# Performance work log

Hardware: AMD Instinct MI355X
Metric: run time of the kernel (lower is better)

## Reference

```python
import jax, jax.numpy as jnp
import numpy as np

M = 262144          # total lanes
N_GROUPS = 32768    # unique obstacle ids (static; original uses torch.unique)
H = 64              # lane_hidden_size
I = 64              # lane_info_enc_size
F = 64              # lane_future_enc_size
SOFT_ARGMAX_DEGREE = 1.0


def setup_inputs() -> dict:
    key = jax.random.key(0)
    k = jax.random.split(key, 8)
    lane_ht = jax.random.normal(k[0], (M, H), jnp.float32)
    lane_info_enc = jax.random.normal(k[1], (M, I), jnp.float32)
    lane_future_enc = jax.random.normal(k[2], (M, F), jnp.float32)
    # sorted group ids covering every group (8 lanes per obstacle)
    same_obstacle_mask = jnp.sort(jnp.arange(M, dtype=jnp.int32) % N_GROUPS).reshape(M, 1)
    # lane_scoring_mlp params: Linear(128->16) + ReLU + Linear(16->1)
    W1 = jax.random.normal(k[3], (H + I, 16), jnp.float32) * 0.05
    b1 = jnp.zeros((16,), jnp.float32)
    W2 = jax.random.normal(k[4], (16, 1), jnp.float32) * 0.05
    b2 = jnp.zeros((1,), jnp.float32)
    return {"lane_ht": lane_ht, "lane_info_enc": lane_info_enc,
            "lane_future_enc": lane_future_enc,
            "W1": W1, "b1": b1, "W2": W2, "b2": b2,
            "same_obstacle_mask": same_obstacle_mask}


def reference(lane_ht, lane_info_enc, lane_future_enc, W1, b1, W2, b2, same_obstacle_mask):
    seg = same_obstacle_mask.reshape(-1)                       # [M] int group ids
    # per-lane score via small MLP
    x = jnp.concatenate([lane_ht, lane_info_enc], axis=1)      # [M, 128]
    h = jax.nn.relu(x @ W1 + b1)                               # [M, 16]
    score = (h @ W2 + b2).reshape(-1) * SOFT_ARGMAX_DEGREE     # [M]
    # per-group (segment) softmax -- exact math of the dense MxN min/max/exp/sum emulation
    smax = jax.lax.stop_gradient(
        jax.ops.segment_max(score, seg, num_segments=N_GROUPS))  # [N]
    e = jnp.exp(score - smax[seg])                             # [M]
    denom = jax.ops.segment_sum(e, seg, num_segments=N_GROUPS)  # [N]
    prob = e / denom[seg]                                      # [M]
    # softmax-weighted per-group pooling of concatenated encodings
    total = jnp.concatenate([lane_ht, lane_info_enc, lane_future_enc], axis=1)  # [M, 192]
    return jax.ops.segment_sum(total * prob[:, None], seg, num_segments=N_GROUPS)  # [N, 192]
```

## Files before the change

kernel.cpp:

```cpp
#include <hip/hip_runtime.h>


__global__ __launch_bounds__(128, 8) void lane_attn_kernel(
    const float* __restrict__ ht,
    const float* __restrict__ info,
    const float* __restrict__ fut,
    const float* __restrict__ W1,
    const float* __restrict__ b1,
    const float* __restrict__ W2,
    const float* __restrict__ b2,
    const int*   __restrict__ seg,
    float*       __restrict__ out)
{
    const int t    = threadIdx.x & 63;
    const int w    = __builtin_amdgcn_readfirstlane(threadIdx.x >> 6);
    const int base = blockIdx.x * 64;

    __shared__ float hpart[2][64][17];

    float h[16];
#pragma unroll
    for (int j = 0; j < 16; ++j) h[j] = w ? 0.0f : b1[j];

    const float*  src = w ? info : ht;
    const float*  w1  = W1 + w * (64 * 16);
    const float4* p   = (const float4*)(src + (size_t)(base + t) * 64);

#pragma unroll 8
    for (int k4 = 0; k4 < 16; ++k4) {
        float4 v = p[k4];
#pragma unroll
        for (int j = 0; j < 16; ++j) {
            h[j] = fmaf(v.x, w1[(k4 * 4 + 0) * 16 + j], h[j]);
            h[j] = fmaf(v.y, w1[(k4 * 4 + 1) * 16 + j], h[j]);
            h[j] = fmaf(v.z, w1[(k4 * 4 + 2) * 16 + j], h[j]);
            h[j] = fmaf(v.w, w1[(k4 * 4 + 3) * 16 + j], h[j]);
        }
    }

#pragma unroll
    for (int j = 0; j < 16; ++j) hpart[w][t][j] = h[j];
    __syncthreads();

    const int lr = w * 32 + (t & 31);
    float score = b2[0];
#pragma unroll
    for (int j = 0; j < 16; ++j) {
        const float hj = hpart[0][lr][j] + hpart[1][lr][j];
        score = fmaf(fmaxf(hj, 0.0f), W2[j], score);
    }

    float m = score;
    m = fmaxf(m, __shfl_xor(m, 1));
    m = fmaxf(m, __shfl_xor(m, 2));
    m = fmaxf(m, __shfl_xor(m, 4));
    float e = __expf(score - m);
    float s = e;
    s += __shfl_xor(s, 1);
    s += __shfl_xor(s, 2);
    s += __shfl_xor(s, 4);
    const float prob = e / s;

    const int c = t;
    for (int gg = 0; gg < 4; ++gg) {
        const int r0  = base + w * 32 + gg * 8;
        const int gid = seg[r0];
        float a0 = 0.0f, a1 = 0.0f, a2 = 0.0f;
#pragma unroll
        for (int i = 0; i < 8; ++i) {
            const float  pb = __shfl(prob, gg * 8 + i);
            const size_t r  = (size_t)(r0 + i) * 64;
            a0 = fmaf(pb, ht[r + c],   a0);
            a1 = fmaf(pb, info[r + c], a1);
            a2 = fmaf(pb, fut[r + c],  a2);
        }
        float* o = out + (size_t)gid * 192;
        o[c]       = a0;
        o[64 + c]  = a1;
        o[128 + c] = a2;
    }
}

extern "C" void kernel_launch(void* const* d_in, const int* in_sizes, int n_in,
                              void* d_out, int out_size, void* d_ws, size_t ws_size,
                              hipStream_t stream) {
    const float* ht   = (const float*)d_in[0];
    const float* info = (const float*)d_in[1];
    const float* fut  = (const float*)d_in[2];
    const float* W1   = (const float*)d_in[3];
    const float* b1   = (const float*)d_in[4];
    const float* W2   = (const float*)d_in[5];
    const float* b2   = (const float*)d_in[6];
    const int*   seg  = (const int*)d_in[7];
    float*       out  = (float*)d_out;

    const int M = in_sizes[7];
    const int blocks = M / 64;

    lane_attn_kernel<<<blocks, 128, 0, stream>>>(ht, info, fut, W1, b1, W2, b2,
                                                 seg, out);
}
```

Before: 215.8 us.

## Stage lane inputs in swizzled LDS tile and split MLP K across four waves

Each block now coalesces its 64 rows of ht and info into a 32KB XOR-swizzled shared-memory tile. The first MLP layer is split across four waves, each owning 32 input features, and the partial sums are reduced through LDS. The pooling step reads ht and info back from LDS instead of re-reading them from global memory, removing the second global pass. The cost is larger LDS use per block, which together with the 256-thread launch bound lowers occupancy.

```diff
diff --git a/kernel.cpp b/kernel.cpp
--- a/kernel.cpp
+++ b/kernel.cpp
@@ -1,7 +1,7 @@
 #include <hip/hip_runtime.h>
 
 
-__global__ __launch_bounds__(128, 8) void lane_attn_kernel(
+__global__ __launch_bounds__(256, 3) void lane_attn_kernel(
     const float* __restrict__ ht,
     const float* __restrict__ info,
     const float* __restrict__ fut,
@@ -12,42 +12,66 @@
     const int*   __restrict__ seg,
     float*       __restrict__ out)
 {
-    const int t    = threadIdx.x & 63;
-    const int w    = __builtin_amdgcn_readfirstlane(threadIdx.x >> 6);
+    const int tid  = threadIdx.x;
+    const int t    = tid & 63;
+    const int w    = __builtin_amdgcn_readfirstlane(tid >> 6);
     const int base = blockIdx.x * 64;
 
-    __shared__ float hpart[2][64][17];
+    __shared__ float4 xtile[64 * 32];
+    __shared__ float  hpart[4][64][20];
+
+#pragma unroll
+    for (int i = 0; i < 8; ++i) {
+        const int g   = i * 256 + tid;
+        const int row = g >> 5;
+        const int s   = g & 31;
+        const float* src = (s < 16)
+            ? (ht   + (size_t)(base + row) * 64 + s * 4)
+            : (info + (size_t)(base + row) * 64 + (s - 16) * 4);
+        xtile[row * 32 + (s ^ (row & 31))] = *(const float4*)src;
+    }
+    __syncthreads();
 
     float h[16];
 #pragma unroll
-    for (int j = 0; j < 16; ++j) h[j] = w ? 0.0f : b1[j];
+    for (int j = 0; j < 16; ++j) h[j] = 0.0f;
 
-    const float*  src = w ? info : ht;
-    const float*  w1  = W1 + w * (64 * 16);
-    const float4* p   = (const float4*)(src + (size_t)(base + t) * 64);
-
-#pragma unroll 8
-    for (int k4 = 0; k4 < 16; ++k4) {
-        float4 v = p[k4];
+    const float* w1 = W1 + (w * 32) * 16;
+#pragma unroll
+    for (int k = 0; k < 8; ++k) {
+        const int s  = w * 8 + k;
+        const float4 v = xtile[t * 32 + (s ^ (t & 31))];
 #pragma unroll
         for (int j = 0; j < 16; ++j) {
-            h[j] = fmaf(v.x, w1[(k4 * 4 + 0) * 16 + j], h[j]);
-            h[j] = fmaf(v.y, w1[(k4 * 4 + 1) * 16 + j], h[j]);
-            h[j] = fmaf(v.z, w1[(k4 * 4 + 2) * 16 + j], h[j]);
-            h[j] = fmaf(v.w, w1[(k4 * 4 + 3) * 16 + j], h[j]);
+            h[j] = fmaf(v.x, w1[(k * 4 + 0) * 16 + j], h[j]);
+            h[j] = fmaf(v.y, w1[(k * 4 + 1) * 16 + j], h[j]);
+            h[j] = fmaf(v.z, w1[(k * 4 + 2) * 16 + j], h[j]);
+            h[j] = fmaf(v.w, w1[(k * 4 + 3) * 16 + j], h[j]);
         }
     }
-
 #pragma unroll
-    for (int j = 0; j < 16; ++j) hpart[w][t][j] = h[j];
+    for (int j4 = 0; j4 < 4; ++j4)
+        *(float4*)&hpart[w][t][j4 * 4] =
+            make_float4(h[j4*4], h[j4*4+1], h[j4*4+2], h[j4*4+3]);
     __syncthreads();
 
-    const int lr = w * 32 + (t & 31);
     float score = b2[0];
+    {
+        float acc[16];
 #pragma unroll
-    for (int j = 0; j < 16; ++j) {
-        const float hj = hpart[0][lr][j] + hpart[1][lr][j];
-        score = fmaf(fmaxf(hj, 0.0f), W2[j], score);
+        for (int j = 0; j < 16; ++j) acc[j] = b1[j];
+#pragma unroll
+        for (int ww = 0; ww < 4; ++ww) {
+#pragma unroll
+            for (int j4 = 0; j4 < 4; ++j4) {
+                const float4 p = *(const float4*)&hpart[ww][t][j4 * 4];
+                acc[j4*4+0] += p.x; acc[j4*4+1] += p.y;
+                acc[j4*4+2] += p.z; acc[j4*4+3] += p.w;
+            }
+        }
+#pragma unroll
+        for (int j = 0; j < 16; ++j)
+            score = fmaf(fmaxf(acc[j], 0.0f), W2[j], score);
     }
 
     float m = score;
@@ -55,29 +79,32 @@
     m = fmaxf(m, __shfl_xor(m, 2));
     m = fmaxf(m, __shfl_xor(m, 4));
     float e = __expf(score - m);
-    float s = e;
-    s += __shfl_xor(s, 1);
-    s += __shfl_xor(s, 2);
-    s += __shfl_xor(s, 4);
-    const float prob = e / s;
+    float s8 = e;
+    s8 += __shfl_xor(s8, 1);
+    s8 += __shfl_xor(s8, 2);
+    s8 += __shfl_xor(s8, 4);
+    const float prob = e / s8;
 
-    const int c = t;
-    for (int gg = 0; gg < 4; ++gg) {
-        const int r0  = base + w * 32 + gg * 8;
-        const int gid = seg[r0];
+    for (int gg = 0; gg < 2; ++gg) {
+        const int g2  = w * 2 + gg;
+        const int r0  = g2 * 8;
+        const int gid = seg[base + r0];
         float a0 = 0.0f, a1 = 0.0f, a2 = 0.0f;
 #pragma unroll
         for (int i = 0; i < 8; ++i) {
-            const float  pb = __shfl(prob, gg * 8 + i);
-            const size_t r  = (size_t)(r0 + i) * 64;
-            a0 = fmaf(pb, ht[r + c],   a0);
-            a1 = fmaf(pb, info[r + c], a1);
-            a2 = fmaf(pb, fut[r + c],  a2);
+            const int   r  = r0 + i;
+            const float p  = __shfl(prob, r);
+            const float* x = (const float*)&xtile[r * 32];
+            const int   s0 = ((t >> 2) ^ (r & 31)) * 4 + (t & 3);
+            const int   s1 = (((t >> 2) + 16) ^ (r & 31)) * 4 + (t & 3);
+            a0 = fmaf(p, x[s0], a0);
+            a1 = fmaf(p, x[s1], a1);
+            a2 = fmaf(p, fut[(size_t)(base + r) * 64 + t], a2);
         }
         float* o = out + (size_t)gid * 192;
-        o[c]       = a0;
-        o[64 + c]  = a1;
-        o[128 + c] = a2;
+        o[t]       = a0;
+        o[64 + t]  = a1;
+        o[128 + t] = a2;
     }
 }
 
@@ -97,6 +124,6 @@
     const int M = in_sizes[7];
     const int blocks = M / 64;
 
-    lane_attn_kernel<<<blocks, 128, 0, stream>>>(ht, info, fut, W1, b1, W2, b2,
+    lane_attn_kernel<<<blocks, 256, 0, stream>>>(ht, info, fut, W1, b1, W2, b2,
                                                  seg, out);
 }
```

Result: no change. 215.2 us (-0.3%).
